# Kernel optimization log

Hardware: AMD Instinct MI355X
Metric: run time of the kernel (lower is better)

Reference implementation:

```python
import jax, jax.numpy as jnp
import numpy as np

STATE_LEN, SEQ_LEN, HIDDEN = 2048, 4096, 2048

def setup_inputs() -> dict:
    key = jax.random.key(0)
    k1, k2, k3, k4 = jax.random.split(key, 4)
    scale = 1.0 / np.sqrt(HIDDEN)
    return {
        "out_state": jax.random.normal(k1, (STATE_LEN, HIDDEN), dtype=jnp.float32),
        "history": jax.random.normal(k2, (SEQ_LEN, HIDDEN), dtype=jnp.float32),
        "W": jax.random.normal(k3, (HIDDEN, HIDDEN), dtype=jnp.float32) * scale,
        "b": jax.random.normal(k4, (HIDDEN,), dtype=jnp.float32) * scale,
    }

def reference(out_state, history, W, b):
    # method='general': energy_j = Linear(history_j) = history_j @ W.T + b
    # score[i, j] = out_state_i . energy_j  -> batched GEMM replacing the double loop
    energies = history @ W.T + b                 # [seq_len, hidden]
    scores = jnp.einsum('ih,jh->ij', out_state, energies)  # [state_len, seq_len]
    # F.softmax on a 2D tensor (legacy default) normalizes over dim=1 (rows)
    return jax.nn.softmax(scores, axis=-1)
```

## Files before the change

### kernel.cpp

```cpp
#include <hip/hip_runtime.h>


#define STATE_LEN 2048
#define SEQ_LEN   4096
#define HIDDEN    2048

#define BM 128
#define BN 128
#define BK 32

typedef __bf16 bf16x8 __attribute__((ext_vector_type(8)));
typedef float f32x4 __attribute__((ext_vector_type(4)));

__device__ __forceinline__ unsigned short f32_to_bf16(float f) {
  unsigned u = __float_as_uint(f);
  u += 0x7FFFu + ((u >> 16) & 1u);
  return (unsigned short)(u >> 16);
}
__device__ __forceinline__ float bf16_to_f32(unsigned short h) {
  return __uint_as_float(((unsigned)h) << 16);
}

__device__ __forceinline__ void gld16(const void* g, void* l) {
  __builtin_amdgcn_global_load_lds(
      (const __attribute__((address_space(1))) unsigned int*)g,
      (__attribute__((address_space(3))) unsigned int*)l,
      16, 0, 0);
}

__global__ __launch_bounds__(256) void split_kernel(
    const float* __restrict__ in, unsigned short* __restrict__ hi,
    unsigned short* __restrict__ lo, int n) {
  int i = (blockIdx.x * 256 + threadIdx.x) * 4;
  if (i >= n) return;
  float4 v = *(const float4*)&in[i];
  ushort4 h, l;
  h.x = f32_to_bf16(v.x); l.x = f32_to_bf16(v.x - bf16_to_f32(h.x));
  h.y = f32_to_bf16(v.y); l.y = f32_to_bf16(v.y - bf16_to_f32(h.y));
  h.z = f32_to_bf16(v.z); l.z = f32_to_bf16(v.z - bf16_to_f32(h.z));
  h.w = f32_to_bf16(v.w); l.w = f32_to_bf16(v.w - bf16_to_f32(h.w));
  *(ushort4*)&hi[i] = h;
  *(ushort4*)&lo[i] = l;
}

__global__ __launch_bounds__(256) void transpose_split_kernel(
    const float* __restrict__ in, unsigned short* __restrict__ hi,
    unsigned short* __restrict__ lo, int rows, int cols) {
  __shared__ float tile[32][33];
  const int bx = blockIdx.x * 32;
  const int by = blockIdx.y * 32;
  const int tx = threadIdx.x;
  const int ty = threadIdx.y;
#pragma unroll
  for (int i = 0; i < 32; i += 8)
    tile[ty + i][tx] = in[(size_t)(by + ty + i) * cols + (bx + tx)];
  __syncthreads();
#pragma unroll
  for (int i = 0; i < 32; i += 8) {
    float x = tile[tx][ty + i];
    unsigned short h = f32_to_bf16(x);
    unsigned short l = f32_to_bf16(x - bf16_to_f32(h));
    size_t o = (size_t)(bx + ty + i) * rows + (by + tx);
    hi[o] = h;
    lo[o] = l;
  }
}

template <bool SPLIT_OUT>
__global__ __launch_bounds__(256, 2) void gemm_bt_split(
    const unsigned short* __restrict__ Ahi, const unsigned short* __restrict__ Alo,
    const unsigned short* __restrict__ Bhi, const unsigned short* __restrict__ Blo,
    float* __restrict__ Cf, unsigned short* __restrict__ Chi,
    unsigned short* __restrict__ Clo, int M, int N, int K) {
  __shared__ __align__(16) unsigned short sAhi[BM * BK];
  __shared__ __align__(16) unsigned short sAlo[BM * BK];
  __shared__ __align__(16) unsigned short sBhi[BN * BK];
  __shared__ __align__(16) unsigned short sBlo[BN * BK];

  const int t = threadIdx.x;
  const int tileM = blockIdx.y * BM;
  const int tileN = blockIdx.x * BN;
  const int rr = t >> 2;
  const int cc = t & 3;

  const int lane = t & 63;
  const int wave = t >> 6;
  const int wm = wave >> 1;
  const int wn = wave & 1;
  const int lr = lane & 15;
  const int kq = (lane >> 4) * 8;

  f32x4 acc[4][4] = {};

  for (int k0 = 0; k0 < K; k0 += BK) {
#pragma unroll
    for (int it = 0; it < 2; ++it) {
      const int r = it * 64 + rr;
      const size_t ga = (size_t)(tileM + r) * K + k0 + cc * 8;
      const size_t gb = (size_t)(tileN + r) * K + k0 + cc * 8;
      const int ls = r * BK + cc * 8;
      gld16(Ahi + ga, &sAhi[ls]);
      gld16(Alo + ga, &sAlo[ls]);
      gld16(Bhi + gb, &sBhi[ls]);
      gld16(Blo + gb, &sBlo[ls]);
    }
    __syncthreads();

    bf16x8 ah[4], al[4], bh[4], bl[4];
#pragma unroll
    for (int mi = 0; mi < 4; ++mi) {
      const int off = (wm * 64 + mi * 16 + lr) * BK + kq;
      ah[mi] = *(const bf16x8*)&sAhi[off];
      al[mi] = *(const bf16x8*)&sAlo[off];
    }
#pragma unroll
    for (int ni = 0; ni < 4; ++ni) {
      const int off = (wn * 64 + ni * 16 + lr) * BK + kq;
      bh[ni] = *(const bf16x8*)&sBhi[off];
      bl[ni] = *(const bf16x8*)&sBlo[off];
    }
#pragma unroll
    for (int mi = 0; mi < 4; ++mi)
#pragma unroll
      for (int ni = 0; ni < 4; ++ni) {
        acc[mi][ni] = __builtin_amdgcn_mfma_f32_16x16x32_bf16(ah[mi], bh[ni], acc[mi][ni], 0, 0, 0);
        acc[mi][ni] = __builtin_amdgcn_mfma_f32_16x16x32_bf16(ah[mi], bl[ni], acc[mi][ni], 0, 0, 0);
        acc[mi][ni] = __builtin_amdgcn_mfma_f32_16x16x32_bf16(al[mi], bh[ni], acc[mi][ni], 0, 0, 0);
      }
    __syncthreads();
  }

#pragma unroll
  for (int mi = 0; mi < 4; ++mi)
#pragma unroll
    for (int ni = 0; ni < 4; ++ni)
#pragma unroll
      for (int e = 0; e < 4; ++e) {
        const int row = tileM + wm * 64 + mi * 16 + (lane >> 4) * 4 + e;
        const int col = tileN + wn * 64 + ni * 16 + lr;
        const float x = acc[mi][ni][e];
        const size_t o = (size_t)row * N + col;
        if (SPLIT_OUT) {
          const unsigned short h = f32_to_bf16(x);
          Chi[o] = h;
          Clo[o] = f32_to_bf16(x - bf16_to_f32(h));
        } else {
          Cf[o] = x;
        }
      }
}

__global__ __launch_bounds__(256) void softmax_rows(float* __restrict__ d, int cols) {
  const int row = blockIdx.x;
  float* p = d + (size_t)row * cols;
  const int t = threadIdx.x;
  const int lane = t & 63;
  const int wave = t >> 6;
  __shared__ float sred[4];

  float4 v[4];
  float m = -3.0e38f;
#pragma unroll
  for (int k = 0; k < 4; ++k) {
    v[k] = *(float4*)&p[(t + k * 256) * 4];
    m = fmaxf(m, fmaxf(fmaxf(v[k].x, v[k].y), fmaxf(v[k].z, v[k].w)));
  }
#pragma unroll
  for (int off = 32; off > 0; off >>= 1) m = fmaxf(m, __shfl_xor(m, off, 64));
  if (lane == 0) sred[wave] = m;
  __syncthreads();
  m = fmaxf(fmaxf(sred[0], sred[1]), fmaxf(sred[2], sred[3]));
  __syncthreads();

  float s = 0.f;
#pragma unroll
  for (int k = 0; k < 4; ++k) {
    v[k].x = __expf(v[k].x - m);
    v[k].y = __expf(v[k].y - m);
    v[k].z = __expf(v[k].z - m);
    v[k].w = __expf(v[k].w - m);
    s += (v[k].x + v[k].y) + (v[k].z + v[k].w);
  }
#pragma unroll
  for (int off = 32; off > 0; off >>= 1) s += __shfl_xor(s, off, 64);
  if (lane == 0) sred[wave] = s;
  __syncthreads();
  s = (sred[0] + sred[1]) + (sred[2] + sred[3]);
  const float inv = 1.0f / s;
#pragma unroll
  for (int k = 0; k < 4; ++k) {
    v[k].x *= inv; v[k].y *= inv; v[k].z *= inv; v[k].w *= inv;
    *(float4*)&p[(t + k * 256) * 4] = v[k];
  }
}

extern "C" void kernel_launch(void* const* d_in, const int* in_sizes, int n_in,
                              void* d_out, int out_size, void* d_ws, size_t ws_size,
                              hipStream_t stream) {
  const float* out_state = (const float*)d_in[0];
  const float* history   = (const float*)d_in[1];
  const float* W         = (const float*)d_in[2];
  float* out = (float*)d_out;

  char* ws = (char*)d_ws;
  const size_t MB = 1ull << 20;
  unsigned short* ohi  = (unsigned short*)(ws + 0 * MB);
  unsigned short* olo  = (unsigned short*)(ws + 8 * MB);
  unsigned short* wthi = (unsigned short*)(ws + 16 * MB);
  unsigned short* wtlo = (unsigned short*)(ws + 24 * MB);
  unsigned short* hhi  = (unsigned short*)(ws + 32 * MB);
  unsigned short* hlo  = (unsigned short*)(ws + 48 * MB);
  unsigned short* thi  = (unsigned short*)(ws + 64 * MB);
  unsigned short* tlo  = (unsigned short*)(ws + 72 * MB);

  split_kernel<<<(STATE_LEN * HIDDEN) / 1024, 256, 0, stream>>>(out_state, ohi, olo,
                                                                STATE_LEN * HIDDEN);
  transpose_split_kernel<<<dim3(HIDDEN / 32, HIDDEN / 32), dim3(32, 8), 0, stream>>>(
      W, wthi, wtlo, HIDDEN, HIDDEN);
  split_kernel<<<(SEQ_LEN * HIDDEN) / 1024, 256, 0, stream>>>(history, hhi, hlo,
                                                              SEQ_LEN * HIDDEN);
  gemm_bt_split<true><<<dim3(HIDDEN / BN, STATE_LEN / BM), 256, 0, stream>>>(
      ohi, olo, wthi, wtlo, nullptr, thi, tlo, STATE_LEN, HIDDEN, HIDDEN);
  gemm_bt_split<false><<<dim3(SEQ_LEN / BN, STATE_LEN / BM), 256, 0, stream>>>(
      thi, tlo, hhi, hlo, out, nullptr, nullptr, STATE_LEN, SEQ_LEN, HIDDEN);
  softmax_rows<<<STATE_LEN, 256, 0, stream>>>(out, SEQ_LEN);
}
```

Measured before the change: 305.6 us.

## Double-buffer GEMM with swizzled LDS, split-K first GEMM, fuse pack kernels

```diff
diff --git a/kernel.cpp b/kernel.cpp
--- a/kernel.cpp
+++ b/kernel.cpp
@@ -8,6 +8,10 @@
 #define BM 128
 #define BN 128
 #define BK 32
+
+#define WAIT_VM8   0x0F78
+#define WAIT_VM0   0x0F70
+#define WAIT_LGKM0 0xC07F
 
 typedef __bf16 bf16x8 __attribute__((ext_vector_type(8)));
 typedef float f32x4 __attribute__((ext_vector_type(4)));
@@ -28,58 +32,98 @@
       16, 0, 0);
 }
 
-__global__ __launch_bounds__(256) void split_kernel(
-    const float* __restrict__ in, unsigned short* __restrict__ hi,
-    unsigned short* __restrict__ lo, int n) {
+__global__ __launch_bounds__(256) void pack_all(
+    const float* __restrict__ os, const float* __restrict__ hist,
+    const float* __restrict__ W,
+    unsigned short* __restrict__ ohi, unsigned short* __restrict__ olo,
+    unsigned short* __restrict__ hhi, unsigned short* __restrict__ hlo,
+    unsigned short* __restrict__ wthi, unsigned short* __restrict__ wtlo) {
+  const int bx = blockIdx.x;
+  const int t = threadIdx.x;
+  if (bx < 12288) {
+    const float* in;
+    unsigned short *hi, *lo;
+    int i;
+    if (bx < 4096) {
+      in = os; hi = ohi; lo = olo; i = (bx * 256 + t) * 4;
+    } else {
+      in = hist; hi = hhi; lo = hlo; i = ((bx - 4096) * 256 + t) * 4;
+    }
+    float4 v = *(const float4*)&in[i];
+    ushort4 h, l;
+    h.x = f32_to_bf16(v.x); l.x = f32_to_bf16(v.x - bf16_to_f32(h.x));
+    h.y = f32_to_bf16(v.y); l.y = f32_to_bf16(v.y - bf16_to_f32(h.y));
+    h.z = f32_to_bf16(v.z); l.z = f32_to_bf16(v.z - bf16_to_f32(h.z));
+    h.w = f32_to_bf16(v.w); l.w = f32_to_bf16(v.w - bf16_to_f32(h.w));
+    *(ushort4*)&hi[i] = h;
+    *(ushort4*)&lo[i] = l;
+  } else {
+    __shared__ float tile[64][65];
+    const int bt = bx - 12288;
+    const int h0 = (bt & 31) * 64;
+    const int k0 = (bt >> 5) * 64;
+    const int lr = t >> 4;
+    const int c4 = (t & 15) * 4;
+#pragma unroll
+    for (int pass = 0; pass < 4; ++pass) {
+      const int row = pass * 16 + lr;
+      float4 v = *(const float4*)&W[(size_t)(h0 + row) * HIDDEN + k0 + c4];
+      tile[row][c4] = v.x; tile[row][c4 + 1] = v.y;
+      tile[row][c4 + 2] = v.z; tile[row][c4 + 3] = v.w;
+    }
+    __syncthreads();
+#pragma unroll
+    for (int pass = 0; pass < 4; ++pass) {
+      const int kl = pass * 16 + (t >> 4);
+      const int hl = (t & 15) * 4;
+      ushort4 h4, l4;
+#pragma unroll
+      for (int j = 0; j < 4; ++j) {
+        const float x = tile[hl + j][kl];
+        const unsigned short h = f32_to_bf16(x);
+        ((unsigned short*)&h4)[j] = h;
+        ((unsigned short*)&l4)[j] = f32_to_bf16(x - bf16_to_f32(h));
+      }
+      const size_t o = (size_t)(k0 + kl) * HIDDEN + h0 + hl;
+      *(ushort4*)&wthi[o] = h4;
+      *(ushort4*)&wtlo[o] = l4;
+    }
+  }
+}
+
+__global__ __launch_bounds__(256) void reduce_split2(
+    const float* __restrict__ p0, const float* __restrict__ p1,
+    unsigned short* __restrict__ hi, unsigned short* __restrict__ lo, int n) {
   int i = (blockIdx.x * 256 + threadIdx.x) * 4;
   if (i >= n) return;
-  float4 v = *(const float4*)&in[i];
+  float4 a = *(const float4*)&p0[i];
+  float4 b = *(const float4*)&p1[i];
+  a.x += b.x; a.y += b.y; a.z += b.z; a.w += b.w;
   ushort4 h, l;
-  h.x = f32_to_bf16(v.x); l.x = f32_to_bf16(v.x - bf16_to_f32(h.x));
-  h.y = f32_to_bf16(v.y); l.y = f32_to_bf16(v.y - bf16_to_f32(h.y));
-  h.z = f32_to_bf16(v.z); l.z = f32_to_bf16(v.z - bf16_to_f32(h.z));
-  h.w = f32_to_bf16(v.w); l.w = f32_to_bf16(v.w - bf16_to_f32(h.w));
+  h.x = f32_to_bf16(a.x); l.x = f32_to_bf16(a.x - bf16_to_f32(h.x));
+  h.y = f32_to_bf16(a.y); l.y = f32_to_bf16(a.y - bf16_to_f32(h.y));
+  h.z = f32_to_bf16(a.z); l.z = f32_to_bf16(a.z - bf16_to_f32(h.z));
+  h.w = f32_to_bf16(a.w); l.w = f32_to_bf16(a.w - bf16_to_f32(h.w));
   *(ushort4*)&hi[i] = h;
   *(ushort4*)&lo[i] = l;
 }
 
-__global__ __launch_bounds__(256) void transpose_split_kernel(
-    const float* __restrict__ in, unsigned short* __restrict__ hi,
-    unsigned short* __restrict__ lo, int rows, int cols) {
-  __shared__ float tile[32][33];
-  const int bx = blockIdx.x * 32;
-  const int by = blockIdx.y * 32;
-  const int tx = threadIdx.x;
-  const int ty = threadIdx.y;
-#pragma unroll
-  for (int i = 0; i < 32; i += 8)
-    tile[ty + i][tx] = in[(size_t)(by + ty + i) * cols + (bx + tx)];
-  __syncthreads();
-#pragma unroll
-  for (int i = 0; i < 32; i += 8) {
-    float x = tile[tx][ty + i];
-    unsigned short h = f32_to_bf16(x);
-    unsigned short l = f32_to_bf16(x - bf16_to_f32(h));
-    size_t o = (size_t)(bx + ty + i) * rows + (by + tx);
-    hi[o] = h;
-    lo[o] = l;
-  }
-}
-
-template <bool SPLIT_OUT>
-__global__ __launch_bounds__(256, 2) void gemm_bt_split(
+template <int KSPLIT>
+__global__ __launch_bounds__(256, 2) void gemm_pipe(
     const unsigned short* __restrict__ Ahi, const unsigned short* __restrict__ Alo,
     const unsigned short* __restrict__ Bhi, const unsigned short* __restrict__ Blo,
-    float* __restrict__ Cf, unsigned short* __restrict__ Chi,
-    unsigned short* __restrict__ Clo, int M, int N, int K) {
-  __shared__ __align__(16) unsigned short sAhi[BM * BK];
-  __shared__ __align__(16) unsigned short sAlo[BM * BK];
-  __shared__ __align__(16) unsigned short sBhi[BN * BK];
-  __shared__ __align__(16) unsigned short sBlo[BN * BK];
+    float* __restrict__ Cf0, float* __restrict__ Cf1, int M, int N, int K) {
+  __shared__ __align__(16) unsigned short sA[2][2][BM * BK];
+  __shared__ __align__(16) unsigned short sB[2][2][BN * BK];
 
   const int t = threadIdx.x;
   const int tileM = blockIdx.y * BM;
   const int tileN = blockIdx.x * BN;
+  const int z = (KSPLIT > 1) ? blockIdx.z : 0;
+  const int kBase = z * (K / KSPLIT);
+  const int iters = (K / KSPLIT) / BK;
+  float* Cf = (KSPLIT > 1 && z == 1) ? Cf1 : Cf0;
+
   const int rr = t >> 2;
   const int cc = t & 3;
 
@@ -88,36 +132,51 @@
   const int wm = wave >> 1;
   const int wn = wave & 1;
   const int lr = lane & 15;
-  const int kq = (lane >> 4) * 8;
+  const int kqc = lane >> 4;
 
   f32x4 acc[4][4] = {};
 
-  for (int k0 = 0; k0 < K; k0 += BK) {
-#pragma unroll
-    for (int it = 0; it < 2; ++it) {
-      const int r = it * 64 + rr;
-      const size_t ga = (size_t)(tileM + r) * K + k0 + cc * 8;
-      const size_t gb = (size_t)(tileN + r) * K + k0 + cc * 8;
+  auto stage = [&](int buf, int k0) {
+#pragma unroll
+    for (int p = 0; p < 2; ++p) {
+      const int r = p * 64 + rr;
+      const int q = cc ^ ((r >> 1) & 3);
+      const size_t ga = (size_t)(tileM + r) * K + k0 + q * 8;
+      const size_t gb = (size_t)(tileN + r) * K + k0 + q * 8;
       const int ls = r * BK + cc * 8;
-      gld16(Ahi + ga, &sAhi[ls]);
-      gld16(Alo + ga, &sAlo[ls]);
-      gld16(Bhi + gb, &sBhi[ls]);
-      gld16(Blo + gb, &sBlo[ls]);
-    }
-    __syncthreads();
+      gld16(Ahi + ga, &sA[buf][0][ls]);
+      gld16(Alo + ga, &sA[buf][1][ls]);
+      gld16(Bhi + gb, &sB[buf][0][ls]);
+      gld16(Blo + gb, &sB[buf][1][ls]);
+    }
+  };
+
+  stage(0, kBase);
+
+  for (int it = 0; it < iters; ++it) {
+    const int buf = it & 1;
+    if (it + 1 < iters) {
+      stage(buf ^ 1, kBase + (it + 1) * BK);
+      __builtin_amdgcn_s_waitcnt(WAIT_VM8);
+    } else {
+      __builtin_amdgcn_s_waitcnt(WAIT_VM0);
+    }
+    __builtin_amdgcn_s_barrier();
 
     bf16x8 ah[4], al[4], bh[4], bl[4];
 #pragma unroll
     for (int mi = 0; mi < 4; ++mi) {
-      const int off = (wm * 64 + mi * 16 + lr) * BK + kq;
-      ah[mi] = *(const bf16x8*)&sAhi[off];
-      al[mi] = *(const bf16x8*)&sAlo[off];
+      const int R = wm * 64 + mi * 16 + lr;
+      const int off = R * BK + (kqc ^ ((R >> 1) & 3)) * 8;
+      ah[mi] = *(const bf16x8*)&sA[buf][0][off];
+      al[mi] = *(const bf16x8*)&sA[buf][1][off];
     }
 #pragma unroll
     for (int ni = 0; ni < 4; ++ni) {
-      const int off = (wn * 64 + ni * 16 + lr) * BK + kq;
-      bh[ni] = *(const bf16x8*)&sBhi[off];
-      bl[ni] = *(const bf16x8*)&sBlo[off];
+      const int R = wn * 64 + ni * 16 + lr;
+      const int off = R * BK + (kqc ^ ((R >> 1) & 3)) * 8;
+      bh[ni] = *(const bf16x8*)&sB[buf][0][off];
+      bl[ni] = *(const bf16x8*)&sB[buf][1][off];
     }
 #pragma unroll
     for (int mi = 0; mi < 4; ++mi)
@@ -127,7 +186,9 @@
         acc[mi][ni] = __builtin_amdgcn_mfma_f32_16x16x32_bf16(ah[mi], bl[ni], acc[mi][ni], 0, 0, 0);
         acc[mi][ni] = __builtin_amdgcn_mfma_f32_16x16x32_bf16(al[mi], bh[ni], acc[mi][ni], 0, 0, 0);
       }
-    __syncthreads();
+
+    __builtin_amdgcn_s_waitcnt(WAIT_LGKM0);
+    __builtin_amdgcn_s_barrier();
   }
 
 #pragma unroll
@@ -138,15 +199,7 @@
       for (int e = 0; e < 4; ++e) {
         const int row = tileM + wm * 64 + mi * 16 + (lane >> 4) * 4 + e;
         const int col = tileN + wn * 64 + ni * 16 + lr;
-        const float x = acc[mi][ni][e];
-        const size_t o = (size_t)row * N + col;
-        if (SPLIT_OUT) {
-          const unsigned short h = f32_to_bf16(x);
-          Chi[o] = h;
-          Clo[o] = f32_to_bf16(x - bf16_to_f32(h));
-        } else {
-          Cf[o] = x;
-        }
+        Cf[(size_t)row * N + col] = acc[mi][ni][e];
       }
 }
 
@@ -210,18 +263,19 @@
   unsigned short* wtlo = (unsigned short*)(ws + 24 * MB);
   unsigned short* hhi  = (unsigned short*)(ws + 32 * MB);
   unsigned short* hlo  = (unsigned short*)(ws + 48 * MB);
-  unsigned short* thi  = (unsigned short*)(ws + 64 * MB);
-  unsigned short* tlo  = (unsigned short*)(ws + 72 * MB);
-
-  split_kernel<<<(STATE_LEN * HIDDEN) / 1024, 256, 0, stream>>>(out_state, ohi, olo,
-                                                                STATE_LEN * HIDDEN);
-  transpose_split_kernel<<<dim3(HIDDEN / 32, HIDDEN / 32), dim3(32, 8), 0, stream>>>(
-      W, wthi, wtlo, HIDDEN, HIDDEN);
-  split_kernel<<<(SEQ_LEN * HIDDEN) / 1024, 256, 0, stream>>>(history, hhi, hlo,
-                                                              SEQ_LEN * HIDDEN);
-  gemm_bt_split<true><<<dim3(HIDDEN / BN, STATE_LEN / BM), 256, 0, stream>>>(
-      ohi, olo, wthi, wtlo, nullptr, thi, tlo, STATE_LEN, HIDDEN, HIDDEN);
-  gemm_bt_split<false><<<dim3(SEQ_LEN / BN, STATE_LEN / BM), 256, 0, stream>>>(
-      thi, tlo, hhi, hlo, out, nullptr, nullptr, STATE_LEN, SEQ_LEN, HIDDEN);
+  float*          pws  = (float*)(ws + 64 * MB);
+  float* g1p0 = pws;
+  float* g1p1 = pws + (size_t)STATE_LEN * HIDDEN;
+  unsigned short* thi = (unsigned short*)(ws + 0 * MB);
+  unsigned short* tlo = (unsigned short*)(ws + 8 * MB);
+
+  pack_all<<<13312, 256, 0, stream>>>(out_state, history, W, ohi, olo, hhi, hlo,
+                                      wthi, wtlo);
+  gemm_pipe<2><<<dim3(HIDDEN / BN, STATE_LEN / BM, 2), 256, 0, stream>>>(
+      ohi, olo, wthi, wtlo, g1p0, g1p1, STATE_LEN, HIDDEN, HIDDEN);
+  reduce_split2<<<(STATE_LEN * HIDDEN) / 1024, 256, 0, stream>>>(
+      g1p0, g1p1, thi, tlo, STATE_LEN * HIDDEN);
+  gemm_pipe<1><<<dim3(SEQ_LEN / BN, STATE_LEN / BM, 1), 256, 0, stream>>>(
+      thi, tlo, hhi, hlo, out, nullptr, STATE_LEN, SEQ_LEN, HIDDEN);
   softmax_rows<<<STATE_LEN, 256, 0, stream>>>(out, SEQ_LEN);
 }
```

New measurement: 273.5 us. 10.5% less time.
